# Optimization experiments

Hardware: AMD Instinct MI355X
Metric: run time of the kernel (lower is better)

The kernel has to match this reference:

```python
import jax, jax.numpy as jnp
import numpy as np

B, T, C, H = 2048, 128, 256, 64

def setup_inputs() -> dict:
    key = jax.random.key(0)
    kx, kk, kq, kv = jax.random.split(key, 4)
    s = 1.0 / np.sqrt(C)  # nn.Linear default init scale (approx)
    return {
        "x": jax.random.normal(kx, (B, T, C), dtype=jnp.float32),
        "Wk": jax.random.uniform(kk, (C, H), jnp.float32, -s, s),
        "Wq": jax.random.uniform(kq, (C, H), jnp.float32, -s, s),
        "Wv": jax.random.uniform(kv, (C, H), jnp.float32, -s, s),
    }

def reference(x, Wk, Wq, Wv):
    # x: [B,T,C]; projections to [B,T,H]
    k = jnp.einsum('btc,ch->bth', x, Wk)
    q = jnp.einsum('btc,ch->bth', x, Wq)
    v = jnp.einsum('btc,ch->bth', x, Wv)
    # NOTE: original scales by C**-0.5 (input dim), not head_size**-0.5
    scale = jnp.asarray(C, x.dtype) ** -0.5
    wei = jnp.einsum('bth,bsh->bts', q, k) * scale  # [B,T,T]
    causal = jnp.tril(jnp.ones((T, T), dtype=bool))
    wei = jnp.where(causal, wei, -jnp.inf)
    wei = jax.nn.softmax(wei, axis=-1)
    # dropout is identity in eval mode (deterministic reference)
    return jnp.einsum('bts,bsh->bth', wei, v)
```

## Files before the change

### kernel.cpp

```cpp
#include <hip/hip_runtime.h>

typedef __bf16 bf16;
typedef __bf16 bf16x4 __attribute__((ext_vector_type(4)));
typedef __bf16 bf16x8 __attribute__((ext_vector_type(8)));
typedef float  f32x4  __attribute__((ext_vector_type(4)));

#define B_ 2048
#define T_ 128
#define C_ 256
#define H_ 64

#define LDX 264
#define LDQ 68
#define LDV 132
#define SMEM_BYTES 67584

__global__ void wt_kernel(const float* __restrict__ Wk, const float* __restrict__ Wq,
                          const float* __restrict__ Wv, bf16* __restrict__ Wt) {
    int o = blockIdx.x * 256 + threadIdx.x;
    int slot = o >> 14;
    int r    = o & 16383;
    int cc   = r >> 6;
    int h    = r & 63;
    const float* src = (slot == 0) ? Wq : (slot == 1 ? Wk : Wv);
    Wt[slot * 16384 + h * 256 + cc] = (bf16)src[r];
}

__global__ void __launch_bounds__(256, 2)
attn_kernel(const float* __restrict__ xg, const bf16* __restrict__ Wt,
            float* __restrict__ outg) {
    __shared__ __align__(16) char smem_raw[SMEM_BYTES];
    bf16* xs  = (bf16*)smem_raw;
    bf16* Qs  = (bf16*)smem_raw;
    bf16* Ks  = (bf16*)(smem_raw + 17408);
    bf16* Vt  = (bf16*)(smem_raw + 34816);
    bf16* Ps  = (bf16*)smem_raw;

    const int tid  = threadIdx.x;
    const int b    = blockIdx.x;
    const int w    = tid >> 6;
    const int lane = tid & 63;
    const int quad = lane >> 4;
    const int n16  = lane & 15;

    const f32x4 zero4 = {0.f, 0.f, 0.f, 0.f};
    const float*  xbp = xg + (size_t)b * (T_ * C_);
    const ushort* WtU = (const ushort*)Wt;

    {
        float4 xa[8], xb4[8];
        #pragma unroll
        for (int i = 0; i < 8; i++) {
            int f = i * 256 + tid;
            xa[i] = *(const float4*)(xbp + (f >> 6) * C_ + (f & 63) * 4);
        }
        #pragma unroll
        for (int g = 0; g < 4; g++) {
            float4* cur = (g & 1) ? xb4 : xa;
            float4* nxt = (g & 1) ? xa : xb4;
            if (g < 3) {
                #pragma unroll
                for (int i = 0; i < 8; i++) {
                    int f = (g + 1) * 2048 + i * 256 + tid;
                    nxt[i] = *(const float4*)(xbp + (f >> 6) * C_ + (f & 63) * 4);
                }
            }
            #pragma unroll
            for (int i = 0; i < 8; i++) {
                int f = g * 2048 + i * 256 + tid;
                int t = f >> 6, c4 = (f & 63) * 4;
                bf16x4 bv = {(bf16)cur[i].x, (bf16)cur[i].y, (bf16)cur[i].z, (bf16)cur[i].w};
                *(bf16x4*)(xs + t * LDX + c4) = bv;
            }
        }
    }
    __syncthreads();

    const int w3 = 3 * w;
    const ushort* wb0 = WtU + ((w3 + 0) >> 2) * 16384 + (16 * ((w3 + 0) & 3) + n16) * 256 + 8 * quad;
    const ushort* wb1 = WtU + ((w3 + 1) >> 2) * 16384 + (16 * ((w3 + 1) & 3) + n16) * 256 + 8 * quad;
    const ushort* wb2 = WtU + ((w3 + 2) >> 2) * 16384 + (16 * ((w3 + 2) & 3) + n16) * 256 + 8 * quad;

    f32x4 acc[8][3];
    #pragma unroll
    for (int mt = 0; mt < 8; mt++)
        #pragma unroll
        for (int j = 0; j < 3; j++) acc[mt][j] = zero4;

    #pragma unroll
    for (int ks = 0; ks < 8; ks++) {
        bf16x8 b0 = *(const bf16x8*)(wb0 + ks * 32);
        bf16x8 b1 = *(const bf16x8*)(wb1 + ks * 32);
        bf16x8 b2 = *(const bf16x8*)(wb2 + ks * 32);
        #pragma unroll
        for (int mt = 0; mt < 8; mt++) {
            bf16x8 a = *(const bf16x8*)(xs + (16 * mt + n16) * LDX + ks * 32 + 8 * quad);
            acc[mt][0] = __builtin_amdgcn_mfma_f32_16x16x32_bf16(a, b0, acc[mt][0], 0, 0, 0);
            acc[mt][1] = __builtin_amdgcn_mfma_f32_16x16x32_bf16(a, b1, acc[mt][1], 0, 0, 0);
            acc[mt][2] = __builtin_amdgcn_mfma_f32_16x16x32_bf16(a, b2, acc[mt][2], 0, 0, 0);
        }
    }
    __syncthreads();

    #pragma unroll
    for (int j = 0; j < 3; j++) {
        int ng = w3 + j;
        if (ng < 4) {
            int h = 16 * ng + n16;
            #pragma unroll
            for (int mt = 0; mt < 8; mt++) {
                int tbase = 16 * mt + 4 * quad;
                #pragma unroll
                for (int r = 0; r < 4; r++)
                    Qs[(tbase + r) * LDQ + h] = (bf16)(acc[mt][j][r] * 0.0625f);
            }
        } else if (ng < 8) {
            int h = 16 * (ng - 4) + n16;
            #pragma unroll
            for (int mt = 0; mt < 8; mt++) {
                int tbase = 16 * mt + 4 * quad;
                #pragma unroll
                for (int r = 0; r < 4; r++)
                    Ks[(tbase + r) * LDQ + h] = (bf16)acc[mt][j][r];
            }
        } else {
            int h = 16 * (ng - 8) + n16;
            #pragma unroll
            for (int mt = 0; mt < 8; mt++) {
                bf16x4 pv = {(bf16)acc[mt][j][0], (bf16)acc[mt][j][1],
                             (bf16)acc[mt][j][2], (bf16)acc[mt][j][3]};
                *(bf16x4*)(Vt + h * LDV + 16 * mt + 4 * quad) = pv;
            }
        }
    }
    __syncthreads();

    f32x4 sacc[2][8];
    int mts[2] = {w, 7 - w};
    #pragma unroll
    for (int half = 0; half < 2; half++) {
        int mt = mts[half];
        int sT = ((mt >> 1) + 1) * 2;
        bf16x8 qa[2];
        #pragma unroll
        for (int ks = 0; ks < 2; ks++)
            qa[ks] = *(const bf16x8*)(Qs + (16 * mt + n16) * LDQ + 32 * ks + 8 * quad);
        #pragma unroll
        for (int nt = 0; nt < 8; nt++) {
            sacc[half][nt] = zero4;
            if (nt < sT) {
                bf16x8 kb0 = *(const bf16x8*)(Ks + (16 * nt + n16) * LDQ + 8 * quad);
                bf16x8 kb1 = *(const bf16x8*)(Ks + (16 * nt + n16) * LDQ + 32 + 8 * quad);
                sacc[half][nt] = __builtin_amdgcn_mfma_f32_16x16x32_bf16(qa[0], kb0, sacc[half][nt], 0, 0, 0);
                sacc[half][nt] = __builtin_amdgcn_mfma_f32_16x16x32_bf16(qa[1], kb1, sacc[half][nt], 0, 0, 0);
            }
        }
        #pragma unroll
        for (int r = 0; r < 4; r++) {
            int t = 16 * mt + 4 * quad + r;
            float mx = -3.0e38f;
            #pragma unroll
            for (int nt = 0; nt < 8; nt++) {
                if (nt < sT) {
                    float v = sacc[half][nt][r];
                    v = (16 * nt + n16 <= t) ? v : -3.0e38f;
                    sacc[half][nt][r] = v;
                    mx = fmaxf(mx, v);
                }
            }
            mx = fmaxf(mx, __shfl_xor(mx, 1));
            mx = fmaxf(mx, __shfl_xor(mx, 2));
            mx = fmaxf(mx, __shfl_xor(mx, 4));
            mx = fmaxf(mx, __shfl_xor(mx, 8));
            float sum = 0.f;
            #pragma unroll
            for (int nt = 0; nt < 8; nt++) {
                if (nt < sT) {
                    float p = __builtin_amdgcn_exp2f((sacc[half][nt][r] - mx) * 1.4426950408889634f);
                    sacc[half][nt][r] = p;
                    sum += p;
                }
            }
            sum += __shfl_xor(sum, 1);
            sum += __shfl_xor(sum, 2);
            sum += __shfl_xor(sum, 4);
            sum += __shfl_xor(sum, 8);
            float rinv = 1.0f / sum;
            #pragma unroll
            for (int nt = 0; nt < 8; nt++)
                if (nt < sT) sacc[half][nt][r] *= rinv;
        }
    }
    __syncthreads();

    #pragma unroll
    for (int half = 0; half < 2; half++) {
        int mt = mts[half];
        int sT = ((mt >> 1) + 1) * 2;
        #pragma unroll
        for (int nt = 0; nt < 8; nt++) {
            if (nt < sT) {
                #pragma unroll
                for (int r = 0; r < 4; r++)
                    Ps[(16 * mt + 4 * quad + r) * LDV + 16 * nt + n16] = (bf16)sacc[half][nt][r];
            }
        }
    }
    __syncthreads();

    #pragma unroll
    for (int half = 0; half < 2; half++) {
        int mt  = mts[half];
        int kst = (mt >> 1) + 1;
        f32x4 oacc[4];
        #pragma unroll
        for (int nt = 0; nt < 4; nt++) oacc[nt] = zero4;
        #pragma unroll
        for (int ks = 0; ks < 4; ks++) {
            if (ks < kst) {
                bf16x8 pa = *(const bf16x8*)(Ps + (16 * mt + n16) * LDV + 32 * ks + 8 * quad);
                #pragma unroll
                for (int nt = 0; nt < 4; nt++) {
                    bf16x8 vb = *(const bf16x8*)(Vt + (16 * nt + n16) * LDV + 32 * ks + 8 * quad);
                    oacc[nt] = __builtin_amdgcn_mfma_f32_16x16x32_bf16(pa, vb, oacc[nt], 0, 0, 0);
                }
            }
        }
        float* ob = outg + ((size_t)b * T_ + 16 * mt + 4 * quad) * H_;
        #pragma unroll
        for (int r = 0; r < 4; r++)
            #pragma unroll
            for (int nt = 0; nt < 4; nt++)
                ob[r * H_ + 16 * nt + n16] = oacc[nt][r];
    }
}

extern "C" void kernel_launch(void* const* d_in, const int* in_sizes, int n_in,
                              void* d_out, int out_size, void* d_ws, size_t ws_size,
                              hipStream_t stream) {
    const float* x  = (const float*)d_in[0];
    const float* Wk = (const float*)d_in[1];
    const float* Wq = (const float*)d_in[2];
    const float* Wv = (const float*)d_in[3];
    bf16* Wt = (bf16*)d_ws;
    wt_kernel<<<192, 256, 0, stream>>>(Wk, Wq, Wv, Wt);
    attn_kernel<<<B_, 256, 0, stream>>>(x, Wt, (float*)d_out);
}
```

Measured before the change: 433.8 us.

## Stream x in 64-column chunks with double-buffered LDS overlapping projection MFMAs

Replaces the full 128x256 bf16 staging of x in shared memory with two 128x64 chunk buffers. The next chunk's global loads are issued before the current chunk's MFMAs, then converted and stored into the alternate buffer. This cuts LDS per block from about 66KB to about 50KB, so launch bounds are raised to 3 blocks per CU, and global latency is hidden behind compute. In exchange it adds a barrier per chunk and puts register pressure on the 96 accumulators plus prefetch registers at the higher occupancy target, which may cause spills.

```diff
diff --git a/kernel.cpp b/kernel.cpp
--- a/kernel.cpp
+++ b/kernel.cpp
@@ -10,10 +10,10 @@
 #define C_ 256
 #define H_ 64
 
-#define LDX 264
+#define LDXC 68
 #define LDQ 68
 #define LDV 132
-#define SMEM_BYTES 67584
+#define SMEM_BYTES 51712
 
 __global__ void wt_kernel(const float* __restrict__ Wk, const float* __restrict__ Wq,
                           const float* __restrict__ Wv, bf16* __restrict__ Wt) {
@@ -26,11 +26,12 @@
     Wt[slot * 16384 + h * 256 + cc] = (bf16)src[r];
 }
 
-__global__ void __launch_bounds__(256, 2)
+__global__ void __launch_bounds__(256, 3)
 attn_kernel(const float* __restrict__ xg, const bf16* __restrict__ Wt,
             float* __restrict__ outg) {
     __shared__ __align__(16) char smem_raw[SMEM_BYTES];
-    bf16* xs  = (bf16*)smem_raw;
+    bf16* cb0 = (bf16*)smem_raw;
+    bf16* cb1 = (bf16*)(smem_raw + 17408);
     bf16* Qs  = (bf16*)smem_raw;
     bf16* Ks  = (bf16*)(smem_raw + 17408);
     bf16* Vt  = (bf16*)(smem_raw + 34816);
@@ -47,32 +48,14 @@
     const float*  xbp = xg + (size_t)b * (T_ * C_);
     const ushort* WtU = (const ushort*)Wt;
 
-    {
-        float4 xa[8], xb4[8];
-        #pragma unroll
-        for (int i = 0; i < 8; i++) {
-            int f = i * 256 + tid;
-            xa[i] = *(const float4*)(xbp + (f >> 6) * C_ + (f & 63) * 4);
-        }
-        #pragma unroll
-        for (int g = 0; g < 4; g++) {
-            float4* cur = (g & 1) ? xb4 : xa;
-            float4* nxt = (g & 1) ? xa : xb4;
-            if (g < 3) {
-                #pragma unroll
-                for (int i = 0; i < 8; i++) {
-                    int f = (g + 1) * 2048 + i * 256 + tid;
-                    nxt[i] = *(const float4*)(xbp + (f >> 6) * C_ + (f & 63) * 4);
-                }
-            }
-            #pragma unroll
-            for (int i = 0; i < 8; i++) {
-                int f = g * 2048 + i * 256 + tid;
-                int t = f >> 6, c4 = (f & 63) * 4;
-                bf16x4 bv = {(bf16)cur[i].x, (bf16)cur[i].y, (bf16)cur[i].z, (bf16)cur[i].w};
-                *(bf16x4*)(xs + t * LDX + c4) = bv;
-            }
-        }
+
+    #pragma unroll
+    for (int i = 0; i < 8; i++) {
+        int f = i * 256 + tid;
+        int t = f >> 4, cc = (f & 15) * 4;
+        float4 v = *(const float4*)(xbp + t * C_ + cc);
+        bf16x4 bv = {(bf16)v.x, (bf16)v.y, (bf16)v.z, (bf16)v.w};
+        *(bf16x4*)(cb0 + t * LDXC + cc) = bv;
     }
     __syncthreads();
 
@@ -88,19 +71,43 @@
         for (int j = 0; j < 3; j++) acc[mt][j] = zero4;
 
     #pragma unroll
-    for (int ks = 0; ks < 8; ks++) {
-        bf16x8 b0 = *(const bf16x8*)(wb0 + ks * 32);
-        bf16x8 b1 = *(const bf16x8*)(wb1 + ks * 32);
-        bf16x8 b2 = *(const bf16x8*)(wb2 + ks * 32);
-        #pragma unroll
-        for (int mt = 0; mt < 8; mt++) {
-            bf16x8 a = *(const bf16x8*)(xs + (16 * mt + n16) * LDX + ks * 32 + 8 * quad);
-            acc[mt][0] = __builtin_amdgcn_mfma_f32_16x16x32_bf16(a, b0, acc[mt][0], 0, 0, 0);
-            acc[mt][1] = __builtin_amdgcn_mfma_f32_16x16x32_bf16(a, b1, acc[mt][1], 0, 0, 0);
-            acc[mt][2] = __builtin_amdgcn_mfma_f32_16x16x32_bf16(a, b2, acc[mt][2], 0, 0, 0);
-        }
-    }
-    __syncthreads();
+    for (int c = 0; c < 4; c++) {
+        bf16* rb = (c & 1) ? cb1 : cb0;
+        bf16* sb = (c & 1) ? cb0 : cb1;
+        float4 pf[8];
+        if (c < 3) {
+            #pragma unroll
+            for (int i = 0; i < 8; i++) {
+                int f = i * 256 + tid;
+                int t = f >> 4, cc = (f & 15) * 4;
+                pf[i] = *(const float4*)(xbp + t * C_ + (c + 1) * 64 + cc);
+            }
+        }
+        #pragma unroll
+        for (int kk = 0; kk < 2; kk++) {
+            int kg = c * 64 + kk * 32;
+            bf16x8 b0 = *(const bf16x8*)(wb0 + kg);
+            bf16x8 b1 = *(const bf16x8*)(wb1 + kg);
+            bf16x8 b2 = *(const bf16x8*)(wb2 + kg);
+            #pragma unroll
+            for (int mt = 0; mt < 8; mt++) {
+                bf16x8 a = *(const bf16x8*)(rb + (16 * mt + n16) * LDXC + kk * 32 + 8 * quad);
+                acc[mt][0] = __builtin_amdgcn_mfma_f32_16x16x32_bf16(a, b0, acc[mt][0], 0, 0, 0);
+                acc[mt][1] = __builtin_amdgcn_mfma_f32_16x16x32_bf16(a, b1, acc[mt][1], 0, 0, 0);
+                acc[mt][2] = __builtin_amdgcn_mfma_f32_16x16x32_bf16(a, b2, acc[mt][2], 0, 0, 0);
+            }
+        }
+        if (c < 3) {
+            #pragma unroll
+            for (int i = 0; i < 8; i++) {
+                int f = i * 256 + tid;
+                int t = f >> 4, cc = (f & 15) * 4;
+                bf16x4 bv = {(bf16)pf[i].x, (bf16)pf[i].y, (bf16)pf[i].z, (bf16)pf[i].w};
+                *(bf16x4*)(sb + t * LDXC + cc) = bv;
+            }
+        }
+        __syncthreads();
+    }
 
     #pragma unroll
     for (int j = 0; j < 3; j++) {
```

New measurement: 460.8 us. 6.2% more time.
